# Performance work log

Hardware: AMD Instinct MI355X
Metric: run time of the kernel (lower is better)

The kernel has to match this reference:

```python
import jax, jax.numpy as jnp
import numpy as np
import math

HEAD_DIM = 128
N_HEADS = 32
N_KV_HEADS = 8
ROPE_THETA = 10000.0


def _rotate_half(x):
    x1, x2 = jnp.split(x, 2, axis=-1)
    return jnp.concatenate([-x2, x1], axis=-1)


def _rope_cos_sin(position_ids, head_dim, theta):
    # position_ids: [B, S] int
    inv_freq = 1.0 / (theta ** (jnp.arange(0, head_dim, 2, dtype=jnp.float32) / head_dim))
    freqs = position_ids.astype(jnp.float32)[..., None] * inv_freq[None, None, :]  # [B,S,D/2]
    emb = jnp.concatenate([freqs, freqs], axis=-1)  # [B,S,D]
    return jnp.cos(emb), jnp.sin(emb)


def setup_inputs() -> dict:
    key = jax.random.key(0)
    k1, k2, k3, k4, k5 = jax.random.split(key, 5)
    B, S, H = 1, 2048, 4096
    hidden_states = jax.random.normal(k1, (B, S, H), dtype=jnp.float32)
    Wq = jax.random.normal(k2, (N_HEADS * HEAD_DIM, H), dtype=jnp.float32) * (1.0 / math.sqrt(H))
    Wk = jax.random.normal(k3, (N_KV_HEADS * HEAD_DIM, H), dtype=jnp.float32) * (1.0 / math.sqrt(H))
    Wv = jax.random.normal(k4, (N_KV_HEADS * HEAD_DIM, H), dtype=jnp.float32) * (1.0 / math.sqrt(H))
    Wo = jax.random.normal(k5, (H, N_HEADS * HEAD_DIM), dtype=jnp.float32) * (1.0 / math.sqrt(H))
    position_ids = jnp.arange(S, dtype=jnp.int32)[None, :]
    return {"hidden_states": hidden_states, "Wq": Wq, "Wk": Wk, "Wv": Wv, "Wo": Wo,
            "position_ids": position_ids}


def reference(hidden_states, Wq, Wk, Wv, Wo, position_ids):
    B, S, H = hidden_states.shape
    d = HEAD_DIM
    groups = N_HEADS // N_KV_HEADS

    # projections (torch Linear: x @ W^T)
    q = (hidden_states @ Wq.T).reshape(B, S, N_HEADS, d).transpose(0, 2, 1, 3)      # [B,Hq,S,d]
    k = (hidden_states @ Wk.T).reshape(B, S, N_KV_HEADS, d).transpose(0, 2, 1, 3)   # [B,Hk,S,d]
    v = (hidden_states @ Wv.T).reshape(B, S, N_KV_HEADS, d).transpose(0, 2, 1, 3)

    cos, sin = _rope_cos_sin(position_ids, d, ROPE_THETA)  # [B,S,d]
    cos = cos[:, None, :, :]
    sin = sin[:, None, :, :]
    q = q * cos + _rotate_half(q) * sin
    k = k * cos + _rotate_half(k) * sin

    # GQA: repeat kv heads
    k = jnp.repeat(k, groups, axis=1)  # [B,Hq,S,d]
    v = jnp.repeat(v, groups, axis=1)

    scores = jnp.einsum('bhqd,bhkd->bhqk', q, k) / math.sqrt(d)
    causal = jnp.tril(jnp.ones((S, S), dtype=bool))
    scores = jnp.where(causal[None, None], scores, jnp.finfo(jnp.float32).min)
    attn = jax.nn.softmax(scores.astype(jnp.float32), axis=-1).astype(q.dtype)

    out = jnp.einsum('bhqk,bhkd->bhqd', attn, v)        # [B,Hq,S,d]
    out = out.transpose(0, 2, 1, 3).reshape(B, S, N_HEADS * d)
    return out @ Wo.T
```

## Files before the change

### kernel.cpp

```cpp
#include <hip/hip_runtime.h>
#include <hip/hip_bf16.h>
#include <cstdint>
#include <cstddef>

#define S_LEN 2048
#define HID   4096
#define HD    128
#define NH    32
#define NKV   8
#define KVW   (NKV * HD)
#define QKVN  (HID + 2 * KVW)

typedef __bf16 bf16x8_t __attribute__((ext_vector_type(8)));
typedef float  f32x4_t  __attribute__((ext_vector_type(4)));
typedef unsigned short u16x8_t __attribute__((ext_vector_type(8)));

__device__ __forceinline__ unsigned short f2b(float f) {
  unsigned u = __float_as_uint(f);
  u += 0x7FFFu + ((u >> 16) & 1u);
  return (unsigned short)(u >> 16);
}
__device__ __forceinline__ float b2f(unsigned short v) {
  return __uint_as_float(((unsigned)v) << 16);
}
__device__ __forceinline__ void gld_lds16(const void* g, void* l) {
  __builtin_amdgcn_global_load_lds(
      (const __attribute__((address_space(1))) void*)g,
      (__attribute__((address_space(3))) void*)l, 16, 0, 0);
}

__global__ void cvt_kernel(const float* __restrict__ src,
                           unsigned short* __restrict__ dst, int n4) {
  int i = blockIdx.x * blockDim.x + threadIdx.x;
  int stride = gridDim.x * blockDim.x;
  for (; i < n4; i += stride) {
    float4 v = reinterpret_cast<const float4*>(src)[i];
    ushort4 o;
    o.x = f2b(v.x); o.y = f2b(v.y); o.z = f2b(v.z); o.w = f2b(v.w);
    reinterpret_cast<ushort4*>(dst)[i] = o;
  }
}

__global__ void rope_kernel(unsigned short* __restrict__ Q,
                            unsigned short* __restrict__ Kb,
                            const int* __restrict__ pos_ids) {
  const int total = S_LEN * (NH + NKV) * 64;
  int idx = blockIdx.x * blockDim.x + threadIdx.x;
  int stride = gridDim.x * blockDim.x;
  for (; idx < total; idx += stride) {
    int s   = idx / ((NH + NKV) * 64);
    int rem = idx % ((NH + NKV) * 64);
    int hp  = rem >> 6;
    int i   = rem & 63;
    unsigned short* ptr; int W, h;
    if (hp < NH) { ptr = Q;  W = HID; h = hp; }
    else         { ptr = Kb; W = KVW; h = hp - NH; }
    float pos = (float)pos_ids[s];
    float ang = pos * __expf(-(float)i * 0.14391156516f);
    float sn, cs;
    sincosf(ang, &sn, &cs);
    size_t base = (size_t)s * W + (size_t)h * HD + i;
    float lo = b2f(ptr[base]);
    float hi = b2f(ptr[base + 64]);
    ptr[base]      = f2b(lo * cs - hi * sn);
    ptr[base + 64] = f2b(hi * cs + lo * sn);
  }
}

template <int BM, int MODE>
__global__ __launch_bounds__(512, 2) void gemm8_kernel(
    const unsigned short* __restrict__ A, const unsigned short* __restrict__ B,
    void* __restrict__ C0, void* __restrict__ C1, void* __restrict__ C2,
    int N, int K) {
  constexpr int BN = 256;
  constexpr int MF = BM / 32;
  constexpr int A_BYTES = BM * 32 * 2;
  constexpr int TILE_BYTES = A_BYTES + BN * 32 * 2;
  constexpr int NLOADS = TILE_BYTES / 8192;
  __shared__ unsigned short lds[4 * (TILE_BYTES / 2)];

  const int tid  = threadIdx.x;
  const int lane = tid & 63;
  const int wid  = tid >> 6;
  const int wm = wid >> 2, wn = wid & 3;
  const int lr = lane & 15, g = lane >> 4;
  const int bm = blockIdx.y * BM;
  const int bn = blockIdx.x * BN;
  const int nt = K >> 5;

  const int cof = (g * 16) ^ ((lr & 6) << 3);

  auto stage_j = [&](int t, int j) {
    const int L = j * 8192 + wid * 1024 + lane * 16;
    const char* src;
    if (L < A_BYTES) {
      const int row = L >> 6;
      const int colb = (L & 63) ^ ((row & 6) << 3);
      src = (const char*)A + ((size_t)(bm + row) * K + t * 32) * 2 + colb;
    } else {
      const int LB = L - A_BYTES;
      const int row = LB >> 6;
      const int colb = (LB & 63) ^ ((row & 6) << 3);
      src = (const char*)B + ((size_t)(bn + row) * K + t * 32) * 2 + colb;
    }
    char* dst = (char*)lds + (t & 3) * TILE_BYTES + L;
    gld_lds16(src, dst);
  };

#pragma unroll
  for (int t = 0; t < 3; ++t)
#pragma unroll
    for (int j = 0; j < NLOADS; ++j) stage_j(t, j);
  asm volatile("s_waitcnt vmcnt(%0)" :: "n"(2 * NLOADS) : "memory");
  __builtin_amdgcn_sched_barrier(0);
  __builtin_amdgcn_s_barrier();

  f32x4_t acc[MF][4];
#pragma unroll
  for (int m = 0; m < MF; ++m)
#pragma unroll
    for (int n = 0; n < 4; ++n) acc[m][n] = f32x4_t{0.f, 0.f, 0.f, 0.f};

  for (int t = 0; t < nt; ++t) {
    const char* base = (const char*)lds + (t & 3) * TILE_BYTES;

    if (t + 3 < nt) {
#pragma unroll
      for (int j = 0; j < NLOADS; ++j) stage_j(t + 3, j);
    }

    bf16x8_t af[MF], bfr[4];
#pragma unroll
    for (int m = 0; m < MF; ++m)
      af[m] = *(const bf16x8_t*)(base + (wm * (BM / 2) + m * 16 + lr) * 64 + cof);
#pragma unroll
    for (int n = 0; n < 4; ++n)
      bfr[n] = *(const bf16x8_t*)(base + A_BYTES + (wn * 64 + n * 16 + lr) * 64 + cof);
    asm volatile("s_waitcnt lgkmcnt(0)" ::: "memory");
    __builtin_amdgcn_sched_barrier(0);

    __builtin_amdgcn_s_setprio(1);
#pragma unroll
    for (int m = 0; m < MF; ++m)
#pragma unroll
      for (int n = 0; n < 4; ++n)
        acc[m][n] = __builtin_amdgcn_mfma_f32_16x16x32_bf16(af[m], bfr[n], acc[m][n], 0, 0, 0);
    __builtin_amdgcn_s_setprio(0);
    __builtin_amdgcn_sched_barrier(0);

    if (t < nt - 3) {
      asm volatile("s_waitcnt vmcnt(%0)" :: "n"(2 * NLOADS) : "memory");
    } else if (t == nt - 3) {
      asm volatile("s_waitcnt vmcnt(%0)" :: "n"(NLOADS) : "memory");
    } else if (t == nt - 2) {
      asm volatile("s_waitcnt vmcnt(0)" ::: "memory");
    }
    __builtin_amdgcn_sched_barrier(0);
    __builtin_amdgcn_s_barrier();
  }

#pragma unroll
  for (int mf = 0; mf < MF; ++mf) {
    const int row0 = bm + wm * (BM / 2) + mf * 16 + g * 4;
#pragma unroll
    for (int nf = 0; nf < 4; ++nf) {
      const int col = bn + wn * 64 + nf * 16 + lr;
      if constexpr (MODE == 1) {
#pragma unroll
        for (int r = 0; r < 4; ++r)
          ((float*)C0)[(size_t)(row0 + r) * N + col] = acc[mf][nf][r];
      } else {
        if (col < HID) {
#pragma unroll
          for (int r = 0; r < 4; ++r)
            ((unsigned short*)C0)[(size_t)(row0 + r) * HID + col] = f2b(acc[mf][nf][r]);
        } else if (col < HID + KVW) {
#pragma unroll
          for (int r = 0; r < 4; ++r)
            ((unsigned short*)C1)[(size_t)(row0 + r) * KVW + (col - HID)] = f2b(acc[mf][nf][r]);
        } else {
          const int c2 = col - HID - KVW;
          ushort4 w;
          w.x = f2b(acc[mf][nf][0]); w.y = f2b(acc[mf][nf][1]);
          w.z = f2b(acc[mf][nf][2]); w.w = f2b(acc[mf][nf][3]);
          *(ushort4*)(void*)&((unsigned short*)C2)[(size_t)c2 * S_LEN + row0] = w;
        }
      }
    }
  }
}

__global__ __launch_bounds__(256) void attn_kernel(
    const unsigned short* __restrict__ Q, const unsigned short* __restrict__ K,
    const unsigned short* __restrict__ VtG, unsigned short* __restrict__ O) {
  __shared__ unsigned short Kl[64][136];
  __shared__ unsigned short Vt[128][72];
  __shared__ unsigned short Pl[4][16][72];

  const int tid  = threadIdx.x;
  const int lane = tid & 63;
  const int wave = tid >> 6;
  const int h    = blockIdx.y;
  const int kvh  = h >> 2;
  const int pair = blockIdx.x;
  const int lr   = lane & 15;
  const int g    = lane >> 4;
  const int lk8  = g * 8;
  const float scale = 0.08838834764831845f;
  const unsigned short* Vbase = VtG + (size_t)kvh * HD * S_LEN;

  const int ksr = tid >> 4, ksc = (tid & 15) * 8;
  const int vsr = tid >> 3, vsc = (tid & 7) * 8;

  for (int pass = 0; pass < 2; ++pass) {
    const int qb = pass == 0 ? (31 - pair) : pair;
    const int q0 = qb * 64;
    const int qrow = q0 + wave * 16;
    const int nkv = qb + 1;

    bf16x8_t qf[4];
    {
      const unsigned short* qp = Q + (size_t)(qrow + lr) * HID + (size_t)h * HD;
#pragma unroll
      for (int c = 0; c < 4; ++c)
        qf[c] = *(const bf16x8_t*)(const void*)(qp + c * 32 + lk8);
    }
    f32x4_t oacc[8];
#pragma unroll
    for (int c = 0; c < 8; ++c) oacc[c] = f32x4_t{0.f, 0.f, 0.f, 0.f};
    float m_run = -3e38f, l_run = 0.f;

    u16x8_t kr[4], vr[4];
#pragma unroll
    for (int i = 0; i < 4; ++i)
      kr[i] = *(const u16x8_t*)(const void*)(K + (size_t)(ksr + i * 16) * KVW +
                                             (size_t)kvh * HD + ksc);
#pragma unroll
    for (int i = 0; i < 4; ++i)
      vr[i] = *(const u16x8_t*)(const void*)(Vbase + (size_t)(vsr + i * 32) * S_LEN + vsc);

    for (int it = 0; it < nkv; ++it) {
      const int kv0 = it * 64;
      __builtin_amdgcn_s_barrier();
#pragma unroll
      for (int i = 0; i < 4; ++i)
        *(u16x8_t*)(void*)&Kl[ksr + i * 16][ksc] = kr[i];
#pragma unroll
      for (int i = 0; i < 4; ++i)
        *(u16x8_t*)(void*)&Vt[vsr + i * 32][vsc] = vr[i];
      if (it + 1 < nkv) {
        const int kn = kv0 + 64;
#pragma unroll
        for (int i = 0; i < 4; ++i)
          kr[i] = *(const u16x8_t*)(const void*)(K + (size_t)(kn + ksr + i * 16) * KVW +
                                                 (size_t)kvh * HD + ksc);
#pragma unroll
        for (int i = 0; i < 4; ++i)
          vr[i] = *(const u16x8_t*)(const void*)(Vbase + (size_t)(vsr + i * 32) * S_LEN +
                                                 kn + vsc);
      }
      asm volatile("s_waitcnt lgkmcnt(0)" ::: "memory");
      __builtin_amdgcn_sched_barrier(0);
      __builtin_amdgcn_s_barrier();

      f32x4_t sacc[4];
#pragma unroll
      for (int n = 0; n < 4; ++n) sacc[n] = f32x4_t{0.f, 0.f, 0.f, 0.f};
#pragma unroll
      for (int c = 0; c < 4; ++c) {
        bf16x8_t qc = qf[c];
#pragma unroll
        for (int n = 0; n < 4; ++n) {
          bf16x8_t kf = *(const bf16x8_t*)(const void*)&Kl[n * 16 + lr][c * 32 + lk8];
          sacc[n] = __builtin_amdgcn_mfma_f32_16x16x32_bf16(kf, qc, sacc[n], 0, 0, 0);
        }
      }

      const int qg = qrow + lr;
      const bool diag = (it == nkv - 1);
      float p[16];
      float mloc = -3e38f;
#pragma unroll
      for (int n = 0; n < 4; ++n)
#pragma unroll
        for (int r = 0; r < 4; ++r) {
          float x = sacc[n][r] * scale;
          if (diag) {
            int kg = kv0 + n * 16 + g * 4 + r;
            if (kg > qg) x = -3e38f;
          }
          p[n * 4 + r] = x;
          mloc = fmaxf(mloc, x);
        }
      mloc = fmaxf(mloc, __shfl_xor(mloc, 16));
      mloc = fmaxf(mloc, __shfl_xor(mloc, 32));

      if (__any(mloc > m_run + 8.f)) {
        float m_new = fmaxf(m_run, mloc);
        float alpha = __expf(m_run - m_new);
        float a4[4];
#pragma unroll
        for (int r = 0; r < 4; ++r) a4[r] = __shfl(alpha, g * 4 + r);
#pragma unroll
        for (int c = 0; c < 8; ++c)
#pragma unroll
          for (int r = 0; r < 4; ++r) oacc[c][r] *= a4[r];
        l_run *= alpha;
        m_run = m_new;
      }

      float ssum = 0.f;
#pragma unroll
      for (int i = 0; i < 16; ++i) {
        float e = __expf(p[i] - m_run);
        p[i] = e;
        ssum += e;
      }
      ssum += __shfl_xor(ssum, 16);
      ssum += __shfl_xor(ssum, 32);
      l_run += ssum;

#pragma unroll
      for (int n = 0; n < 4; ++n) {
        ushort4 w;
        w.x = f2b(p[n * 4 + 0]); w.y = f2b(p[n * 4 + 1]);
        w.z = f2b(p[n * 4 + 2]); w.w = f2b(p[n * 4 + 3]);
        *(ushort4*)(void*)&Pl[wave][lr][n * 16 + g * 4] = w;
      }

#pragma unroll
      for (int half = 0; half < 2; ++half) {
        bf16x8_t pf = *(const bf16x8_t*)(const void*)&Pl[wave][lr][half * 32 + lk8];
#pragma unroll
        for (int c = 0; c < 8; ++c) {
          bf16x8_t vf = *(const bf16x8_t*)(const void*)&Vt[c * 16 + lr][half * 32 + lk8];
          oacc[c] = __builtin_amdgcn_mfma_f32_16x16x32_bf16(pf, vf, oacc[c], 0, 0, 0);
        }
      }
    }

    float linv[4];
#pragma unroll
    for (int r = 0; r < 4; ++r) linv[r] = 1.f / __shfl(l_run, g * 4 + r);
#pragma unroll
    for (int r = 0; r < 4; ++r) {
      int row = qrow + g * 4 + r;
#pragma unroll
      for (int c = 0; c < 8; ++c)
        O[(size_t)row * HID + (size_t)h * HD + c * 16 + lr] = f2b(oacc[c][r] * linv[r]);
    }
  }
}

extern "C" void kernel_launch(void* const* d_in, const int* in_sizes, int n_in,
                              void* d_out, int out_size, void* d_ws, size_t ws_size,
                              hipStream_t stream) {
  (void)in_sizes; (void)n_in; (void)out_size; (void)ws_size;
  const float* X  = (const float*)d_in[0];
  const float* Wq = (const float*)d_in[1];
  const float* Wk = (const float*)d_in[2];
  const float* Wv = (const float*)d_in[3];
  const float* Wo = (const float*)d_in[4];
  const int*  pos = (const int*)d_in[5];
  float* out = (float*)d_out;

  unsigned short* Xb  = (unsigned short*)d_ws;
  unsigned short* Wqb = Xb  + (size_t)S_LEN * HID;
  unsigned short* Wkb = Wqb + (size_t)HID * HID;
  unsigned short* Wvb = Wkb + (size_t)KVW * HID;
  unsigned short* Wob = Wvb + (size_t)KVW * HID;
  unsigned short* Qb  = Wob + (size_t)HID * HID;
  unsigned short* Kb  = Qb  + (size_t)S_LEN * HID;
  unsigned short* VtB = Kb  + (size_t)S_LEN * KVW;
  unsigned short* AOb = VtB + (size_t)S_LEN * KVW;

  auto cvt = [&](const float* s, unsigned short* d, size_t n) {
    int n4 = (int)(n / 4);
    int grid = (n4 + 255) / 256;
    if (grid > 4096) grid = 4096;
    cvt_kernel<<<grid, 256, 0, stream>>>(s, d, n4);
  };
  cvt(X,  Xb,  (size_t)S_LEN * HID);
  cvt(Wq, Wqb, (size_t)HID * HID);
  cvt(Wk, Wkb, (size_t)KVW * HID);
  cvt(Wv, Wvb, (size_t)KVW * HID);
  cvt(Wo, Wob, (size_t)HID * HID);

  gemm8_kernel<256, 2><<<dim3(QKVN / 256, S_LEN / 256), 512, 0, stream>>>(
      Xb, Wqb, Qb, Kb, VtB, QKVN, HID);

  rope_kernel<<<2048, 256, 0, stream>>>(Qb, Kb, pos);

  attn_kernel<<<dim3(16, NH), 256, 0, stream>>>(Qb, Kb, VtB, AOb);

  gemm8_kernel<128, 1><<<dim3(HID / 256, S_LEN / 128), 512, 0, stream>>>(
      AOb, Wob, out, nullptr, nullptr, HID, HID);
}
```

Measured before the change: 325.3 us.

## Restructure GEMM into ping-pong pipeline with K=64 tiles and block swizzle

The GEMM kernel now uses two LDS buffers holding K=64 tiles instead of four K=32 buffers. Each tile is split into four MFMA sub-blocks, and global-to-LDS loads for upcoming tiles are interleaved between them under barriers, so memory traffic overlaps with matrix math. It also remaps workgroup IDs with an 8-way XCD-style swizzle to improve L2 locality, and widens the LDS XOR swizzle to 128-byte rows. The cost is more barriers and tighter hand-managed vmcnt accounting, which risks stalls or ordering mistakes.

```diff
diff --git a/kernel.cpp b/kernel.cpp
--- a/kernel.cpp
+++ b/kernel.cpp
@@ -68,100 +68,180 @@
 }
 
 template <int BM, int MODE>
-__global__ __launch_bounds__(512, 2) void gemm8_kernel(
+__global__ __launch_bounds__(512, 2) void gemm8p_kernel(
     const unsigned short* __restrict__ A, const unsigned short* __restrict__ B,
     void* __restrict__ C0, void* __restrict__ C1, void* __restrict__ C2,
     int N, int K) {
   constexpr int BN = 256;
-  constexpr int MF = BM / 32;
-  constexpr int A_BYTES = BM * 32 * 2;
-  constexpr int TILE_BYTES = A_BYTES + BN * 32 * 2;
-  constexpr int NLOADS = TILE_BYTES / 8192;
-  __shared__ unsigned short lds[4 * (TILE_BYTES / 2)];
+  constexpr int PWM = BM / 2;
+  constexpr int MFR = PWM / 16;
+  constexpr int MPP = MFR / 4;
+  constexpr int ABYTES = BM * 128;
+  constexpr int TILE_LDS = ABYTES + BN * 128;
+  constexpr int A_UNITS = ABYTES / 8192;
+  constexpr int TUNITS = A_UNITS + 4;
+  constexpr int VM_N = TUNITS - 2;
+  __shared__ char ldsB[2 * TILE_LDS];
 
   const int tid  = threadIdx.x;
   const int lane = tid & 63;
   const int wid  = tid >> 6;
   const int wm = wid >> 2, wn = wid & 3;
   const int lr = lane & 15, g = lane >> 4;
-  const int bm = blockIdx.y * BM;
-  const int bn = blockIdx.x * BN;
-  const int nt = K >> 5;
-
-  const int cof = (g * 16) ^ ((lr & 6) << 3);
-
-  auto stage_j = [&](int t, int j) {
-    const int L = j * 8192 + wid * 1024 + lane * 16;
+
+  const int gx = gridDim.x;
+  const int nwg = gx * gridDim.y;
+  const int lin = blockIdx.y * gx + blockIdx.x;
+  const int swz = (lin & 7) * (nwg >> 3) + (lin >> 3);
+  const int bm = (swz / gx) * BM;
+  const int bn = (swz % gx) * BN;
+
+  const int nk = K >> 6;
+  const int ni = nk >> 1;
+  const int xr = (lr & 7) << 4;
+
+  auto stage_u = [&](int t, int u) {
+    if (t >= nk) return;
+    const int riu = tid >> 3;
+    const int cbs = ((tid & 7) << 4) ^ ((riu & 7) << 4);
     const char* src;
-    if (L < A_BYTES) {
-      const int row = L >> 6;
-      const int colb = (L & 63) ^ ((row & 6) << 3);
-      src = (const char*)A + ((size_t)(bm + row) * K + t * 32) * 2 + colb;
-    } else {
-      const int LB = L - A_BYTES;
-      const int row = LB >> 6;
-      const int colb = (LB & 63) ^ ((row & 6) << 3);
-      src = (const char*)B + ((size_t)(bn + row) * K + t * 32) * 2 + colb;
-    }
-    char* dst = (char*)lds + (t & 3) * TILE_BYTES + L;
-    gld_lds16(src, dst);
+    if (u < A_UNITS)
+      src = (const char*)A + ((size_t)(bm + u * 64 + riu) * K + t * 64) * 2 + cbs;
+    else
+      src = (const char*)B + ((size_t)(bn + (u - A_UNITS) * 64 + riu) * K + t * 64) * 2 + cbs;
+    gld_lds16(src, ldsB + (t & 1) * TILE_LDS + u * 8192 + tid * 16);
   };
 
-#pragma unroll
-  for (int t = 0; t < 3; ++t)
-#pragma unroll
-    for (int j = 0; j < NLOADS; ++j) stage_j(t, j);
-  asm volatile("s_waitcnt vmcnt(%0)" :: "n"(2 * NLOADS) : "memory");
+  auto rdA = [&](const char* bb, int m, int k) {
+    const int row = wm * PWM + m * 16 + lr;
+    return *(const bf16x8_t*)(bb + row * 128 + ((k * 64 + g * 16) ^ xr));
+  };
+  auto rdB = [&](const char* bb, int n, int k) {
+    const int row = wn * 64 + n * 16 + lr;
+    return *(const bf16x8_t*)(bb + ABYTES + row * 128 + ((k * 64 + g * 16) ^ xr));
+  };
+
+  for (int t = 0; t < 2; ++t)
+    for (int u = 0; u < TUNITS; ++u) stage_u(t, u);
+  asm volatile("s_waitcnt vmcnt(0)" ::: "memory");
   __builtin_amdgcn_sched_barrier(0);
   __builtin_amdgcn_s_barrier();
 
-  f32x4_t acc[MF][4];
-#pragma unroll
-  for (int m = 0; m < MF; ++m)
+  f32x4_t acc[MFR][4];
+#pragma unroll
+  for (int m = 0; m < MFR; ++m)
 #pragma unroll
     for (int n = 0; n < 4; ++n) acc[m][n] = f32x4_t{0.f, 0.f, 0.f, 0.f};
 
-  for (int t = 0; t < nt; ++t) {
-    const char* base = (const char*)lds + (t & 3) * TILE_BYTES;
-
-    if (t + 3 < nt) {
-#pragma unroll
-      for (int j = 0; j < NLOADS; ++j) stage_j(t + 3, j);
+  bf16x8_t bfr[4][2], af[MPP][2];
+
+#define MFMA_BLOCK(MB)                                                        \
+  __builtin_amdgcn_s_setprio(1);                                              \
+  _Pragma("unroll") for (int m = 0; m < MPP; ++m)                             \
+    _Pragma("unroll") for (int n = 0; n < 4; ++n)                             \
+      _Pragma("unroll") for (int k = 0; k < 2; ++k)                           \
+        acc[(MB) + m][n] = __builtin_amdgcn_mfma_f32_16x16x32_bf16(           \
+            af[m][k], bfr[n][k], acc[(MB) + m][n], 0, 0, 0);                  \
+  __builtin_amdgcn_s_setprio(0);
+
+#define GATE()                                                                \
+  __builtin_amdgcn_s_barrier();                                               \
+  asm volatile("s_waitcnt lgkmcnt(0)" ::: "memory");                          \
+  __builtin_amdgcn_sched_barrier(0);
+
+  for (int i = 0; i < ni; ++i) {
+    const char* baseE = ldsB;
+    const char* baseO = ldsB + TILE_LDS;
+    const int tO = 2 * i + 1, tE2 = 2 * i + 2, tO2 = 2 * i + 3;
+    const bool last = (i == ni - 1);
+
+#pragma unroll
+    for (int n = 0; n < 4; ++n)
+#pragma unroll
+      for (int k = 0; k < 2; ++k) bfr[n][k] = rdB(baseE, n, k);
+#pragma unroll
+    for (int m = 0; m < MPP; ++m)
+#pragma unroll
+      for (int k = 0; k < 2; ++k) af[m][k] = rdA(baseE, m, k);
+    if (i > 0) {
+      if constexpr (BM == 256) { stage_u(tO, 1); stage_u(tO, 3); }
+      else                     { stage_u(tO, 0); stage_u(tO, 1); }
     }
-
-    bf16x8_t af[MF], bfr[4];
-#pragma unroll
-    for (int m = 0; m < MF; ++m)
-      af[m] = *(const bf16x8_t*)(base + (wm * (BM / 2) + m * 16 + lr) * 64 + cof);
+    GATE(); MFMA_BLOCK(0);
+    __builtin_amdgcn_s_barrier();
+
+#pragma unroll
+    for (int m = 0; m < MPP; ++m)
+#pragma unroll
+      for (int k = 0; k < 2; ++k) af[m][k] = rdA(baseE, MPP + m, k);
+    stage_u(tE2, A_UNITS + 0); stage_u(tE2, A_UNITS + 1);
+    GATE(); MFMA_BLOCK(MPP);
+    __builtin_amdgcn_s_barrier();
+
+#pragma unroll
+    for (int m = 0; m < MPP; ++m)
+#pragma unroll
+      for (int k = 0; k < 2; ++k) af[m][k] = rdA(baseE, 2 * MPP + m, k);
+    stage_u(tE2, A_UNITS + 2); stage_u(tE2, A_UNITS + 3);
+    GATE(); MFMA_BLOCK(2 * MPP);
+    __builtin_amdgcn_s_barrier();
+
+#pragma unroll
+    for (int m = 0; m < MPP; ++m)
+#pragma unroll
+      for (int k = 0; k < 2; ++k) af[m][k] = rdA(baseE, 3 * MPP + m, k);
+    if constexpr (BM == 256) { stage_u(tE2, 0); stage_u(tE2, 2); }
+    GATE(); MFMA_BLOCK(3 * MPP);
+    if (last) { asm volatile("s_waitcnt vmcnt(0)" ::: "memory"); }
+    else      { asm volatile("s_waitcnt vmcnt(%0)" :: "n"(VM_N) : "memory"); }
+    __builtin_amdgcn_sched_barrier(0);
+    __builtin_amdgcn_s_barrier();
+
 #pragma unroll
     for (int n = 0; n < 4; ++n)
-      bfr[n] = *(const bf16x8_t*)(base + A_BYTES + (wn * 64 + n * 16 + lr) * 64 + cof);
-    asm volatile("s_waitcnt lgkmcnt(0)" ::: "memory");
+#pragma unroll
+      for (int k = 0; k < 2; ++k) bfr[n][k] = rdB(baseO, n, k);
+#pragma unroll
+    for (int m = 0; m < MPP; ++m)
+#pragma unroll
+      for (int k = 0; k < 2; ++k) af[m][k] = rdA(baseO, m, k);
+    if constexpr (BM == 256) { stage_u(tE2, 1); stage_u(tE2, 3); }
+    else                     { stage_u(tE2, 0); stage_u(tE2, 1); }
+    GATE(); MFMA_BLOCK(0);
+    __builtin_amdgcn_s_barrier();
+
+#pragma unroll
+    for (int m = 0; m < MPP; ++m)
+#pragma unroll
+      for (int k = 0; k < 2; ++k) af[m][k] = rdA(baseO, MPP + m, k);
+    stage_u(tO2, A_UNITS + 0); stage_u(tO2, A_UNITS + 1);
+    GATE(); MFMA_BLOCK(MPP);
+    __builtin_amdgcn_s_barrier();
+
+#pragma unroll
+    for (int m = 0; m < MPP; ++m)
+#pragma unroll
+      for (int k = 0; k < 2; ++k) af[m][k] = rdA(baseO, 2 * MPP + m, k);
+    stage_u(tO2, A_UNITS + 2); stage_u(tO2, A_UNITS + 3);
+    GATE(); MFMA_BLOCK(2 * MPP);
+    __builtin_amdgcn_s_barrier();
+
+#pragma unroll
+    for (int m = 0; m < MPP; ++m)
+#pragma unroll
+      for (int k = 0; k < 2; ++k) af[m][k] = rdA(baseO, 3 * MPP + m, k);
+    if constexpr (BM == 256) { stage_u(tO2, 0); stage_u(tO2, 2); }
+    GATE(); MFMA_BLOCK(3 * MPP);
+    if (!last) { asm volatile("s_waitcnt vmcnt(%0)" :: "n"(VM_N) : "memory"); }
     __builtin_amdgcn_sched_barrier(0);
-
-    __builtin_amdgcn_s_setprio(1);
-#pragma unroll
-    for (int m = 0; m < MF; ++m)
-#pragma unroll
-      for (int n = 0; n < 4; ++n)
-        acc[m][n] = __builtin_amdgcn_mfma_f32_16x16x32_bf16(af[m], bfr[n], acc[m][n], 0, 0, 0);
-    __builtin_amdgcn_s_setprio(0);
-    __builtin_amdgcn_sched_barrier(0);
-
-    if (t < nt - 3) {
-      asm volatile("s_waitcnt vmcnt(%0)" :: "n"(2 * NLOADS) : "memory");
-    } else if (t == nt - 3) {
-      asm volatile("s_waitcnt vmcnt(%0)" :: "n"(NLOADS) : "memory");
-    } else if (t == nt - 2) {
-      asm volatile("s_waitcnt vmcnt(0)" ::: "memory");
-    }
-    __builtin_amdgcn_sched_barrier(0);
     __builtin_amdgcn_s_barrier();
   }
-
-#pragma unroll
-  for (int mf = 0; mf < MF; ++mf) {
-    const int row0 = bm + wm * (BM / 2) + mf * 16 + g * 4;
+#undef MFMA_BLOCK
+#undef GATE
+
+#pragma unroll
+  for (int mf = 0; mf < MFR; ++mf) {
+    const int row0 = bm + wm * PWM + mf * 16 + g * 4;
 #pragma unroll
     for (int nf = 0; nf < 4; ++nf) {
       const int col = bn + wn * 64 + nf * 16 + lr;
@@ -386,13 +466,13 @@
   cvt(Wv, Wvb, (size_t)KVW * HID);
   cvt(Wo, Wob, (size_t)HID * HID);
 
-  gemm8_kernel<256, 2><<<dim3(QKVN / 256, S_LEN / 256), 512, 0, stream>>>(
+  gemm8p_kernel<256, 2><<<dim3(QKVN / 256, S_LEN / 256), 512, 0, stream>>>(
       Xb, Wqb, Qb, Kb, VtB, QKVN, HID);
 
   rope_kernel<<<2048, 256, 0, stream>>>(Qb, Kb, pos);
 
   attn_kernel<<<dim3(16, NH), 256, 0, stream>>>(Qb, Kb, VtB, AOb);
 
-  gemm8_kernel<128, 1><<<dim3(HID / 256, S_LEN / 128), 512, 0, stream>>>(
+  gemm8p_kernel<128, 1><<<dim3(HID / 256, S_LEN / 128), 512, 0, stream>>>(
       AOb, Wob, out, nullptr, nullptr, HID, HID);
 }
```

New measurement: 334.5 us. 1.03x slower.
